# Optimization experiments

Measured on AMD Instinct MI355X. Metric: run time of the kernel, lower is better.

Reference implementation:

```python
import jax, jax.numpy as jnp
import numpy as np

N = 200000      # active voxels
K = 27          # kernel volume (3x3x3)
M = 50000       # rulebook pairs per kernel offset
CIN = 64
COUT = 64


def setup_inputs() -> dict:
    key = jax.random.key(0)
    k1, k2, k3, k4 = jax.random.split(key, 4)
    feats = jax.random.normal(k1, (N, CIN), dtype=jnp.float32)
    std = 1.0 / np.sqrt(CIN * K)
    kernel = jax.random.uniform(k2, (K, CIN, COUT), dtype=jnp.float32,
                                minval=-std, maxval=std)
    in_map = jax.random.randint(k3, (K, M), 0, N, dtype=jnp.int32)
    out_map = jax.random.randint(k4, (K, M), 0, N, dtype=jnp.int32)
    return {"feats": feats, "kernel": kernel, "in_map": in_map, "out_map": out_map}


def reference(feats, kernel, in_map, out_map):
    # gather: [K, M, Cin]
    gathered = feats[in_map]
    # per-offset GEMM: [K, M, Cout]
    partial = jnp.einsum('kmi,kio->kmo', gathered, kernel)
    # scatter-add into output features [N, Cout]
    out = jnp.zeros((feats.shape[0], kernel.shape[-1]), dtype=feats.dtype)
    out = out.at[out_map].add(partial)
    return out
```

## Files before the change

### kernel.cpp

```cpp
#include <hip/hip_runtime.h>
#include <hip/hip_fp16.h>

#define CIN   64
#define COUT  64

typedef __attribute__((ext_vector_type(8))) short bf16x8;
typedef __attribute__((ext_vector_type(4))) float f32x4;

__device__ inline unsigned short f2bf(float f) {
    unsigned u = __float_as_uint(f);
    return (unsigned short)((u + 0x7FFFu + ((u >> 16) & 1u)) >> 16);
}

__device__ inline unsigned pack_h2(float lo, float hi) {
    __half l = __float2half(lo), h = __float2half(hi);
    return (unsigned)__half_as_ushort(l) | ((unsigned)__half_as_ushort(h) << 16);
}

__device__ inline float2 h2f2(unsigned v) {
    return make_float2(
        __half2float(__ushort_as_half((unsigned short)(v & 0xFFFFu))),
        __half2float(__ushort_as_half((unsigned short)(v >> 16))));
}

__global__ __launch_bounds__(256)
void cvt_hist(const float4* __restrict__ in, unsigned short* __restrict__ outb,
              int n8, const int* __restrict__ out_map, int total,
              int* __restrict__ cnt, int* __restrict__ rk) {
    int i = blockIdx.x * 256 + threadIdx.x;
    if (i < n8) {
        float4 f0 = in[2 * i], f1 = in[2 * i + 1];
        bf16x8 o;
        o[0] = (short)f2bf(f0.x); o[1] = (short)f2bf(f0.y);
        o[2] = (short)f2bf(f0.z); o[3] = (short)f2bf(f0.w);
        o[4] = (short)f2bf(f1.x); o[5] = (short)f2bf(f1.y);
        o[6] = (short)f2bf(f1.z); o[7] = (short)f2bf(f1.w);
        *(bf16x8*)(outb + 8 * (size_t)i) = o;
    }
    if (i < total)
        rk[i] = atomicAdd(&cnt[out_map[i]], 1);
}

__global__ __launch_bounds__(256)
void scanA(const int* __restrict__ cnt, int* __restrict__ excl,
           int* __restrict__ blocksum, int N) {
    __shared__ int sm[256];
    const int b = blockIdx.x, t = threadIdx.x;
    const int base = b * 1024 + t * 4;
    int v0 = (base + 0 < N) ? cnt[base + 0] : 0;
    int v1 = (base + 1 < N) ? cnt[base + 1] : 0;
    int v2 = (base + 2 < N) ? cnt[base + 2] : 0;
    int v3 = (base + 3 < N) ? cnt[base + 3] : 0;
    const int s = v0 + v1 + v2 + v3;
    sm[t] = s; __syncthreads();
    for (int off = 1; off < 256; off <<= 1) {
        int x = (t >= off) ? sm[t - off] : 0;
        __syncthreads();
        sm[t] += x;
        __syncthreads();
    }
    const int e = sm[t] - s;
    if (t == 255) blocksum[b] = sm[t];
    if (base + 0 < N) excl[base + 0] = e;
    if (base + 1 < N) excl[base + 1] = e + v0;
    if (base + 2 < N) excl[base + 2] = e + v0 + v1;
    if (base + 3 < N) excl[base + 3] = e + v0 + v1 + v2;
}

__global__ __launch_bounds__(256)
void scanB(const int* __restrict__ blocksum, int* __restrict__ blockbase,
           int nb, int* __restrict__ total_out) {
    __shared__ int sm[256];
    const int t = threadIdx.x;
    const int s = (t < nb) ? blocksum[t] : 0;
    sm[t] = s; __syncthreads();
    for (int off = 1; off < 256; off <<= 1) {
        int x = (t >= off) ? sm[t - off] : 0;
        __syncthreads();
        sm[t] += x;
        __syncthreads();
    }
    if (t < nb) blockbase[t] = sm[t] - s;
    if (t == 255) *total_out = sm[255];
}

__global__ __launch_bounds__(256)
void scanC(int* __restrict__ offsets, const int* __restrict__ blockbase, int N) {
    int i = blockIdx.x * 256 + threadIdx.x;
    if (i >= N) return;
    offsets[i] += blockbase[i >> 10];
}

__global__ __launch_bounds__(256)
void spconv_phase1(const unsigned short* __restrict__ featsb,
                   const float*          __restrict__ weight,
                   const int*            __restrict__ in_map,
                   const int*            __restrict__ out_map,
                   const int*            __restrict__ offsets,
                   const int*            __restrict__ rk,
                   unsigned*             __restrict__ partial_dw,
                   int M) {
    const int k      = blockIdx.y;
    const int tid    = threadIdx.x;
    const int lane   = tid & 63;
    const int m      = lane & 15;
    const int quad   = lane >> 4;
    const int wave   = blockIdx.x * 4 + (tid >> 6);
    const int nwaves = gridDim.x * 4;

    const float* __restrict__ wk = weight + (size_t)k * (CIN * COUT);
    bf16x8 afrag[4][2];
#pragma unroll
    for (int t = 0; t < 4; ++t) {
        const int n = 16 * (m >> 2) + 4 * t + (m & 3);
#pragma unroll
        for (int h = 0; h < 2; ++h) {
            const int c0 = 32 * h + 8 * quad;
#pragma unroll
            for (int j = 0; j < 8; ++j)
                afrag[t][h][j] = (short)f2bf(wk[(c0 + j) * COUT + n]);
        }
    }

    const int base   = k * M;
    const int ntiles = M >> 4;

    int t0 = wave, t1 = wave + nwaves, t2 = wave + 2 * nwaves;

    int ir0 = 0, orow0 = 0, rk0 = 0;
    if (t0 < ntiles) {
        const int p = base + (t0 << 4) + m;
        ir0 = in_map[p]; orow0 = out_map[p]; rk0 = rk[p];
    }
    int slt0 = 0; bf16x8 a0_0 = {}, a1_0 = {};
    if (t0 < ntiles) {
        if (quad == 0) slt0 = offsets[orow0] + rk0;
        const unsigned short* fb = featsb + ((size_t)ir0 << 6) + 8 * quad;
        a0_0 = *(const bf16x8*)fb;
        a1_0 = *(const bf16x8*)(fb + 32);
    }
    int ir1 = 0, orow1 = 0, rk1 = 0;
    if (t1 < ntiles) {
        const int p = base + (t1 << 4) + m;
        ir1 = in_map[p]; orow1 = out_map[p]; rk1 = rk[p];
    }

    while (t0 < ntiles) {
        int slt1 = 0; bf16x8 a0_1 = {}, a1_1 = {};
        if (t1 < ntiles) {
            if (quad == 0) slt1 = offsets[orow1] + rk1;
            const unsigned short* fb = featsb + ((size_t)ir1 << 6) + 8 * quad;
            a0_1 = *(const bf16x8*)fb;
            a1_1 = *(const bf16x8*)(fb + 32);
        }
        int ir2 = 0, orow2 = 0, rk2 = 0;
        if (t2 < ntiles) {
            const int p = base + (t2 << 4) + m;
            ir2 = in_map[p]; orow2 = out_map[p]; rk2 = rk[p];
        }

        f32x4 acc[4];
#pragma unroll
        for (int t = 0; t < 4; ++t) {
            acc[t] = {0.f, 0.f, 0.f, 0.f};
            acc[t] = __builtin_amdgcn_mfma_f32_16x16x32_bf16(afrag[t][0], a0_0, acc[t], 0, 0, 0);
            acc[t] = __builtin_amdgcn_mfma_f32_16x16x32_bf16(afrag[t][1], a1_0, acc[t], 0, 0, 0);
        }

        const int s = __shfl(slt0, m);
        unsigned d[8];
#pragma unroll
        for (int t = 0; t < 4; ++t) {
            d[2 * t]     = pack_h2(acc[t][0], acc[t][1]);
            d[2 * t + 1] = pack_h2(acc[t][2], acc[t][3]);
        }
        uint4* dst = (uint4*)(partial_dw + (size_t)s * 32 + 8 * quad);
        dst[0] = make_uint4(d[0], d[1], d[2], d[3]);
        dst[1] = make_uint4(d[4], d[5], d[6], d[7]);

        t0 = t1; t1 = t2; t2 += nwaves;
        slt0 = slt1; a0_0 = a0_1; a1_0 = a1_1;
        ir1 = ir2; orow1 = orow2; rk1 = rk2;
    }
}

__global__ __launch_bounds__(256)
void spconv_phase2(const uint4* __restrict__ partial_q,
                   const int*   __restrict__ offsets,
                   float4*      __restrict__ out4,
                   int nrows) {
    const int tid  = threadIdx.x;
    const int lane = tid & 63;
    const int g    = lane >> 3;
    const int q    = lane & 7;
    const int wave = blockIdx.x * 4 + (tid >> 6);
    const int nw   = gridDim.x * 4;

    if (wave >= nrows) return;
    int cur_s = offsets[wave];
    int cur_e = offsets[wave + 1];

    for (int r = wave; r < nrows; r += nw) {
        const int start = cur_s;
        const int c     = cur_e - start;
        const int rn    = r + nw;
        if (rn < nrows) {
            cur_s = offsets[rn];
            cur_e = offsets[rn + 1];
        }

        float s0 = 0.f, s1 = 0.f, s2 = 0.f, s3 = 0.f;
        float s4 = 0.f, s5 = 0.f, s6 = 0.f, s7 = 0.f;
        for (int j0 = 0; j0 < c; j0 += 8) {
            const int j = j0 + g;
            if (j < c) {
                const uint4 v = partial_q[(size_t)(start + j) * 8 + q];
                const float2 f0 = h2f2(v.x), f1 = h2f2(v.y);
                const float2 f2 = h2f2(v.z), f3 = h2f2(v.w);
                s0 += f0.x; s1 += f0.y; s2 += f1.x; s3 += f1.y;
                s4 += f2.x; s5 += f2.y; s6 += f3.x; s7 += f3.y;
            }
        }

#pragma unroll
        for (int msk = 8; msk <= 32; msk <<= 1) {
            s0 += __shfl_xor(s0, msk); s1 += __shfl_xor(s1, msk);
            s2 += __shfl_xor(s2, msk); s3 += __shfl_xor(s3, msk);
            s4 += __shfl_xor(s4, msk); s5 += __shfl_xor(s5, msk);
            s6 += __shfl_xor(s6, msk); s7 += __shfl_xor(s7, msk);
        }

        if (g == 0) {
            out4[(size_t)r * 16 + 2 * q]     = make_float4(s0, s1, s2, s3);
            out4[(size_t)r * 16 + 2 * q + 1] = make_float4(s4, s5, s6, s7);
        }
    }
}

__global__ __launch_bounds__(256)
void spconv_atomic(const float* __restrict__ feats,
                   const float* __restrict__ weight,
                   const int*   __restrict__ in_map,
                   const int*   __restrict__ out_map,
                   float*       __restrict__ out,
                   int M) {
    const int k      = blockIdx.y;
    const int tid    = threadIdx.x;
    const int lane   = tid & 63;
    const int m      = lane & 15;
    const int quad   = lane >> 4;
    const int wave   = blockIdx.x * 4 + (tid >> 6);
    const int nwaves = gridDim.x * 4;

    const float* __restrict__ wk = weight + (size_t)k * (CIN * COUT);
    bf16x8 bfrag[4][2];
#pragma unroll
    for (int t = 0; t < 4; ++t)
#pragma unroll
        for (int h = 0; h < 2; ++h) {
            const int n  = 16 * t + m;
            const int c0 = 32 * h + 8 * quad;
#pragma unroll
            for (int j = 0; j < 8; ++j)
                bfrag[t][h][j] = (short)f2bf(wk[(c0 + j) * COUT + n]);
        }

    const int base   = k * M;
    const int ntiles = M >> 4;

    for (int tile = wave; tile < ntiles; tile += nwaves) {
        const int p0 = tile << 4;
        const int in_row  = in_map[base + p0 + m];
        const int out_row = out_map[base + p0 + m];

        const float* __restrict__ fr = feats + ((size_t)in_row << 6) + 8 * quad;
        const f32x4 f0 = *(const f32x4*)(fr + 0);
        const f32x4 f1 = *(const f32x4*)(fr + 4);
        const f32x4 f2 = *(const f32x4*)(fr + 32);
        const f32x4 f3 = *(const f32x4*)(fr + 36);

        bf16x8 a0, a1;
#pragma unroll
        for (int j = 0; j < 4; ++j) {
            a0[j]     = (short)f2bf(f0[j]);
            a0[j + 4] = (short)f2bf(f1[j]);
            a1[j]     = (short)f2bf(f2[j]);
            a1[j + 4] = (short)f2bf(f3[j]);
        }

        int orow[4];
#pragma unroll
        for (int r = 0; r < 4; ++r)
            orow[r] = __shfl(out_row, 4 * quad + r);

        f32x4 acc[4];
#pragma unroll
        for (int t = 0; t < 4; ++t) {
            acc[t] = {0.f, 0.f, 0.f, 0.f};
            acc[t] = __builtin_amdgcn_mfma_f32_16x16x32_bf16(a0, bfrag[t][0], acc[t], 0, 0, 0);
            acc[t] = __builtin_amdgcn_mfma_f32_16x16x32_bf16(a1, bfrag[t][1], acc[t], 0, 0, 0);
        }

#pragma unroll
        for (int t = 0; t < 4; ++t)
#pragma unroll
            for (int r = 0; r < 4; ++r)
                atomicAdd(out + (size_t)orow[r] * COUT + 16 * t + m, acc[t][r]);
    }
}

__global__ __launch_bounds__(256)
void zero_out_kernel(float4* __restrict__ out, int n4) {
    int i = blockIdx.x * 256 + threadIdx.x;
    if (i < n4) out[i] = make_float4(0.f, 0.f, 0.f, 0.f);
}

static inline size_t al256(size_t x) { return (x + 255) & ~(size_t)255; }

extern "C" void kernel_launch(void* const* d_in, const int* in_sizes, int n_in,
                              void* d_out, int out_size, void* d_ws, size_t ws_size,
                              hipStream_t stream) {
    const float* feats   = (const float*)d_in[0];
    const float* weight  = (const float*)d_in[1];
    const int*   in_map  = (const int*)d_in[2];
    const int*   out_map = (const int*)d_in[3];
    float*       out     = (float*)d_out;

    const int K     = in_sizes[1] / (CIN * COUT);
    const int M     = in_sizes[2] / K;
    const int N     = out_size / COUT;
    const int total = K * M;
    const int nb    = (N + 1023) >> 10;

    const size_t off_b  = al256((size_t)(N + 1) * 4);
    const size_t cnt_b  = al256((size_t)N * 4);
    const size_t bs_b   = al256((size_t)nb * 4);
    const size_t bb_b   = al256((size_t)nb * 4);
    const size_t rank_b = al256((size_t)total * 4);
    const size_t fb_b   = al256((size_t)N * CIN * 2);
    const size_t part_b = (size_t)total * COUT * 2;
    const size_t need   = off_b + cnt_b + bs_b + bb_b + rank_b + fb_b + part_b;

    if ((M & 15) == 0 && nb <= 256 && ws_size >= need) {
        char* p = (char*)d_ws;
        int*            offsets   = (int*)p;            p += off_b;
        int*            cnt       = (int*)p;            p += cnt_b;
        int*            blocksum  = (int*)p;            p += bs_b;
        int*            blockbase = (int*)p;            p += bb_b;
        int*            rk        = (int*)p;            p += rank_b;
        unsigned short* featsb    = (unsigned short*)p; p += fb_b;
        unsigned*       partial   = (unsigned*)p;

        const int n8 = N * CIN / 8;
        const int fused_n = (n8 > total) ? n8 : total;

        hipMemsetAsync(cnt, 0, (size_t)N * 4, stream);
        cvt_hist<<<(fused_n + 255) / 256, 256, 0, stream>>>(
            (const float4*)feats, featsb, n8, out_map, total, cnt, rk);
        scanA<<<nb, 256, 0, stream>>>(cnt, offsets, blocksum, N);
        scanB<<<1, 256, 0, stream>>>(blocksum, blockbase, nb, offsets + N);
        scanC<<<(N + 255) / 256, 256, 0, stream>>>(offsets, blockbase, N);

        dim3 g1(80, K);
        spconv_phase1<<<g1, 256, 0, stream>>>(featsb, weight, in_map, out_map,
                                              offsets, rk, partial, M);

        spconv_phase2<<<8192, 256, 0, stream>>>((const uint4*)partial, offsets,
                                                (float4*)out, N);
        return;
    }

    int n4 = out_size / 4;
    zero_out_kernel<<<(n4 + 255) / 256, 256, 0, stream>>>((float4*)out, n4);
    dim3 grid(80, K);
    spconv_atomic<<<grid, 256, 0, stream>>>(feats, weight, in_map, out_map, out, M);
}
```

Measured before the change: 303.8 us.

## Precompute bf16 weight fragments, double phase1 grid, add nontemporal loads

```diff
diff --git a/kernel.cpp b/kernel.cpp
--- a/kernel.cpp
+++ b/kernel.cpp
@@ -6,6 +6,7 @@
 
 typedef __attribute__((ext_vector_type(8))) short bf16x8;
 typedef __attribute__((ext_vector_type(4))) float f32x4;
+typedef __attribute__((ext_vector_type(4))) unsigned u32x4;
 
 __device__ inline unsigned short f2bf(float f) {
     unsigned u = __float_as_uint(f);
@@ -24,17 +25,18 @@
 }
 
 __global__ __launch_bounds__(256)
-void cvt_hist(const float4* __restrict__ in, unsigned short* __restrict__ outb,
+void cvt_hist(const f32x4* __restrict__ in, unsigned short* __restrict__ outb,
               int n8, const int* __restrict__ out_map, int total,
               int* __restrict__ cnt, int* __restrict__ rk) {
     int i = blockIdx.x * 256 + threadIdx.x;
     if (i < n8) {
-        float4 f0 = in[2 * i], f1 = in[2 * i + 1];
+        f32x4 f0 = __builtin_nontemporal_load(&in[2 * i]);
+        f32x4 f1 = __builtin_nontemporal_load(&in[2 * i + 1]);
         bf16x8 o;
-        o[0] = (short)f2bf(f0.x); o[1] = (short)f2bf(f0.y);
-        o[2] = (short)f2bf(f0.z); o[3] = (short)f2bf(f0.w);
-        o[4] = (short)f2bf(f1.x); o[5] = (short)f2bf(f1.y);
-        o[6] = (short)f2bf(f1.z); o[7] = (short)f2bf(f1.w);
+        o[0] = (short)f2bf(f0[0]); o[1] = (short)f2bf(f0[1]);
+        o[2] = (short)f2bf(f0[2]); o[3] = (short)f2bf(f0[3]);
+        o[4] = (short)f2bf(f1[0]); o[5] = (short)f2bf(f1[1]);
+        o[6] = (short)f2bf(f1[2]); o[7] = (short)f2bf(f1[3]);
         *(bf16x8*)(outb + 8 * (size_t)i) = o;
     }
     if (i < total)
@@ -85,15 +87,31 @@
 }
 
 __global__ __launch_bounds__(256)
-void scanC(int* __restrict__ offsets, const int* __restrict__ blockbase, int N) {
-    int i = blockIdx.x * 256 + threadIdx.x;
-    if (i >= N) return;
-    offsets[i] += blockbase[i >> 10];
-}
-
-__global__ __launch_bounds__(256)
+void scanC(int* __restrict__ offsets, const int* __restrict__ blockbase, int N,
+           int nblk, const float* __restrict__ weight,
+           unsigned short* __restrict__ wb, int kvol) {
+    const int b = blockIdx.x;
+    if (b < nblk) {
+        int i = b * 256 + threadIdx.x;
+        if (i < N) offsets[i] += blockbase[i >> 10];
+        return;
+    }
+    const int idx = (b - nblk) * 256 + threadIdx.x;
+    if (idx >= kvol * 64 * 8) return;
+    const int k   = idx >> 9;
+    const int rem = idx & 511;
+    const int n   = rem >> 3;
+    const int c0  = (rem & 7) << 3;
+    const float* __restrict__ wk = weight + (size_t)k * (CIN * COUT);
+    unsigned short* __restrict__ dst = wb + ((size_t)k * 64 + n) * 64 + c0;
+#pragma unroll
+    for (int j = 0; j < 8; ++j)
+        dst[j] = f2bf(wk[(c0 + j) * COUT + n]);
+}
+
+__global__ __launch_bounds__(256, 8)
 void spconv_phase1(const unsigned short* __restrict__ featsb,
-                   const float*          __restrict__ weight,
+                   const unsigned short* __restrict__ wb,
                    const int*            __restrict__ in_map,
                    const int*            __restrict__ out_map,
                    const int*            __restrict__ offsets,
@@ -108,18 +126,14 @@
     const int wave   = blockIdx.x * 4 + (tid >> 6);
     const int nwaves = gridDim.x * 4;
 
-    const float* __restrict__ wk = weight + (size_t)k * (CIN * COUT);
+    const unsigned short* __restrict__ wkb = wb + (size_t)k * (CIN * COUT);
     bf16x8 afrag[4][2];
 #pragma unroll
     for (int t = 0; t < 4; ++t) {
         const int n = 16 * (m >> 2) + 4 * t + (m & 3);
 #pragma unroll
-        for (int h = 0; h < 2; ++h) {
-            const int c0 = 32 * h + 8 * quad;
-#pragma unroll
-            for (int j = 0; j < 8; ++j)
-                afrag[t][h][j] = (short)f2bf(wk[(c0 + j) * COUT + n]);
-        }
+        for (int h = 0; h < 2; ++h)
+            afrag[t][h] = *(const bf16x8*)(wkb + n * 64 + 32 * h + 8 * quad);
     }
 
     const int base   = k * M;
@@ -185,7 +199,7 @@
 }
 
 __global__ __launch_bounds__(256)
-void spconv_phase2(const uint4* __restrict__ partial_q,
+void spconv_phase2(const u32x4* __restrict__ partial_q,
                    const int*   __restrict__ offsets,
                    float4*      __restrict__ out4,
                    int nrows) {
@@ -214,9 +228,10 @@
         for (int j0 = 0; j0 < c; j0 += 8) {
             const int j = j0 + g;
             if (j < c) {
-                const uint4 v = partial_q[(size_t)(start + j) * 8 + q];
-                const float2 f0 = h2f2(v.x), f1 = h2f2(v.y);
-                const float2 f2 = h2f2(v.z), f3 = h2f2(v.w);
+                const u32x4 v = __builtin_nontemporal_load(
+                    &partial_q[(size_t)(start + j) * 8 + q]);
+                const float2 f0 = h2f2(v[0]), f1 = h2f2(v[1]);
+                const float2 f2 = h2f2(v[2]), f3 = h2f2(v[3]);
                 s0 += f0.x; s1 += f0.y; s2 += f1.x; s3 += f1.y;
                 s4 += f2.x; s5 += f2.y; s6 += f3.x; s7 += f3.y;
             }
@@ -337,9 +352,10 @@
     const size_t bs_b   = al256((size_t)nb * 4);
     const size_t bb_b   = al256((size_t)nb * 4);
     const size_t rank_b = al256((size_t)total * 4);
+    const size_t wb_b   = al256((size_t)K * CIN * COUT * 2);
     const size_t fb_b   = al256((size_t)N * CIN * 2);
     const size_t part_b = (size_t)total * COUT * 2;
-    const size_t need   = off_b + cnt_b + bs_b + bb_b + rank_b + fb_b + part_b;
+    const size_t need   = off_b + cnt_b + bs_b + bb_b + rank_b + wb_b + fb_b + part_b;
 
     if ((M & 15) == 0 && nb <= 256 && ws_size >= need) {
         char* p = (char*)d_ws;
@@ -348,24 +364,29 @@
         int*            blocksum  = (int*)p;            p += bs_b;
         int*            blockbase = (int*)p;            p += bb_b;
         int*            rk        = (int*)p;            p += rank_b;
+        unsigned short* wb        = (unsigned short*)p; p += wb_b;
         unsigned short* featsb    = (unsigned short*)p; p += fb_b;
         unsigned*       partial   = (unsigned*)p;
 
         const int n8 = N * CIN / 8;
         const int fused_n = (n8 > total) ? n8 : total;
 
-        hipMemsetAsync(cnt, 0, (size_t)N * 4, stream);
+        (void)hipMemsetAsync(cnt, 0, (size_t)N * 4, stream);
         cvt_hist<<<(fused_n + 255) / 256, 256, 0, stream>>>(
-            (const float4*)feats, featsb, n8, out_map, total, cnt, rk);
+            (const f32x4*)feats, featsb, n8, out_map, total, cnt, rk);
         scanA<<<nb, 256, 0, stream>>>(cnt, offsets, blocksum, N);
         scanB<<<1, 256, 0, stream>>>(blocksum, blockbase, nb, offsets + N);
-        scanC<<<(N + 255) / 256, 256, 0, stream>>>(offsets, blockbase, N);
-
-        dim3 g1(80, K);
-        spconv_phase1<<<g1, 256, 0, stream>>>(featsb, weight, in_map, out_map,
+
+        const int nblkC = (N + 255) / 256;
+        const int nwblk = (K * 64 * 8 + 255) / 256;
+        scanC<<<nblkC + nwblk, 256, 0, stream>>>(offsets, blockbase, N,
+                                                 nblkC, weight, wb, K);
+
+        dim3 g1(160, K);
+        spconv_phase1<<<g1, 256, 0, stream>>>(featsb, wb, in_map, out_map,
                                               offsets, rk, partial, M);
 
-        spconv_phase2<<<8192, 256, 0, stream>>>((const uint4*)partial, offsets,
+        spconv_phase2<<<8192, 256, 0, stream>>>((const u32x4*)partial, offsets,
                                                 (float4*)out, N);
         return;
     }
```

Measured after the change: 304.0 us. About the same (+0.1%).
